# Optimization experiments

Hardware: AMD Instinct MI355X
Metric: run time of the kernel (lower is better)

## Reference

```python
import jax, jax.numpy as jnp
import numpy as np
import math

B, K, Q = 8, 3000, 256
KDIM = QDIM = ADIM = ODIM = 512
H_MA, H_CA = 4, 1
CHUNK = 16
SHARPEN = 1.0
EPS = 1e-6
INIT_R = -4.0


def setup_inputs() -> dict:
    key = jax.random.key(0)
    ks = jax.random.split(key, 10)
    s = 0.02  # weight scale so sigmoid/softmax operate in a sane range
    return {
        "key": jax.random.normal(ks[0], (B, K, KDIM), jnp.float32),
        "query": jax.random.normal(ks[1], (B, Q, QDIM), jnp.float32),
        "w_key_ma": jax.random.normal(ks[2], (KDIM, ADIM), jnp.float32) * s,
        "b_key_ma": jnp.zeros((ADIM,), jnp.float32),
        "w_query_ma": jax.random.normal(ks[3], (QDIM, ADIM), jnp.float32) * s,
        "b_query_ma": jnp.zeros((ADIM,), jnp.float32),
        "r": jnp.full((H_MA,), INIT_R, jnp.float32),
        "w_key_ca": jax.random.normal(ks[4], (KDIM, ADIM), jnp.float32) * s,
        "b_key_ca": jnp.zeros((ADIM,), jnp.float32),
        "w_query_ca": jax.random.normal(ks[5], (QDIM, ADIM), jnp.float32) * s,
        "b_query_ca": jnp.zeros((ADIM,), jnp.float32),
        "w_value": jax.random.normal(ks[6], (KDIM, ODIM), jnp.float32) * s,
        "b_value": jnp.zeros((ODIM,), jnp.float32),
    }


def _heads(x, n_heads):
    # [B, T, n_heads*d] -> [B, n_heads, T, d]
    b, t, d = x.shape
    return x.reshape(b, t, n_heads, d // n_heads).transpose(0, 2, 1, 3)


def moving_sum(x, back, forward):
    """Moving sum over last axis: out[k] = sum_{j=k-back}^{k+forward} x[j].
    Equivalent to F.conv1d with an all-ones kernel (cumsum-difference form)."""
    w = back + forward + 1
    pad = [(0, 0)] * (x.ndim - 1) + [(back, forward)]
    cs = jnp.cumsum(jnp.pad(x, pad), axis=-1)
    cs = jnp.concatenate([jnp.zeros_like(cs[..., :1]), cs], axis=-1)
    return cs[..., w:] - cs[..., :-w]


def exclusive_cumsum(x):
    # [a,b,c] -> [0,a,a+b] along last axis
    z = jnp.zeros_like(x[..., :1])
    return jnp.cumsum(jnp.concatenate([z, x[..., :-1]], axis=-1), axis=-1)


def safe_cumprod(x, eps):
    # exclusive cumprod via cumsum in log space
    return jnp.exp(exclusive_cumsum(jnp.log(jnp.clip(x, eps, 1.0))))


def monotonic_alpha(p_choose, eps):
    """Parallel (training-time) monotonic attention recurrence over qlen.
    p_choose: [B, H, Q, K] -> alpha: [B, H, Q, K]"""
    cp = safe_cumprod(1.0 - p_choose, eps)          # [B,H,Q,K]
    cp_c = jnp.clip(cp, eps, 1.0)
    # scan over query steps
    p_t = jnp.moveaxis(p_choose, 2, 0)              # [Q,B,H,K]
    cp_t = jnp.moveaxis(cp, 2, 0)
    cpc_t = jnp.moveaxis(cp_c, 2, 0)
    b, h, k = p_choose.shape[0], p_choose.shape[1], p_choose.shape[3]
    a0 = jnp.zeros((b, h, k), p_choose.dtype).at[:, :, 0].set(1.0)  # attend to frame 0

    def step(a_prev, inp):
        p_i, cp_i, cpc_i = inp
        a_i = p_i * cp_i * jnp.cumsum(a_prev / cpc_i, axis=-1)
        return a_i, a_i

    _, alpha_t = jax.lax.scan(step, a0, (p_t, cp_t, cpc_t))
    return jnp.moveaxis(alpha_t, 0, 2)              # [B,H,Q,K]


def efficient_chunkwise_attention(alpha, u, chunk_size, sharpening_factor):
    """alpha: [B,H_ma,Q,K], u: [B,H_ca,Q,K] (shared across MA heads).
    Returns beta: [B, H_ma*H_ca, Q, K]."""
    bs, h_ma, qlen, klen = alpha.shape
    a5 = alpha[:, :, None]                          # [B,H_ma,1,Q,K]
    u5 = u[:, None]                                 # [B,1,H_ca,Q,K]
    u5 = u5 - jnp.max(u5, axis=-1, keepdims=True)
    softmax_exp = jnp.clip(jnp.exp(u5), 1e-5, None)
    denom = moving_sum(softmax_exp, back=chunk_size - 1, forward=0)
    beta = softmax_exp * moving_sum(a5 * sharpening_factor / denom,
                                    back=0, forward=chunk_size - 1)
    return beta.reshape(bs, -1, qlen, klen)


def reference(key, query, w_key_ma, b_key_ma, w_query_ma, b_query_ma, r,
              w_key_ca, b_key_ca, w_query_ca, b_query_ca, w_value, b_value):
    scale = math.sqrt(ADIM)
    # monotonic energy (scaled_dot, H_ma heads) + offset r
    k_ma = _heads(key @ w_key_ma + b_key_ma, H_MA)          # [B,H,K,dk]
    q_ma = _heads(query @ w_query_ma + b_query_ma, H_MA)    # [B,H,Q,dk]
    e_ma = jnp.einsum('bhqd,bhkd->bhqk', q_ma, k_ma) / scale
    e_ma = e_ma + r[None, :, None, None]
    p_choose = jax.nn.sigmoid(e_ma)                          # [B,H_ma,Q,K]

    alpha = monotonic_alpha(p_choose, EPS)                   # [B,H_ma,Q,K]

    # chunk energy (scaled_dot, H_ca heads, shared across MA heads)
    k_ca = _heads(key @ w_key_ca + b_key_ca, H_CA)
    q_ca = _heads(query @ w_query_ca + b_query_ca, H_CA)
    u = jnp.einsum('bhqd,bhkd->bhqk', q_ca, k_ca) / scale    # [B,H_ca,Q,K]

    beta = efficient_chunkwise_attention(alpha, u, CHUNK, SHARPEN)  # [B,H_ma,Q,K]

    # context vector
    v = _heads(key @ w_value + b_value, H_MA * H_CA)         # [B,H,K,dv]
    cv = jnp.einsum('bhqk,bhkd->bhqd', beta, v)              # [B,H,Q,dv]
    cv = cv.transpose(0, 2, 1, 3).reshape(B, Q, ODIM)
    return cv, alpha, beta
```

## Files before the change

kernel.cpp:

```cpp
#include <hip/hip_runtime.h>
#include <hip/hip_bf16.h>
#include <math.h>

#define EPSV 1e-6f
#define INV_SCALE 0.04419417382415922f

typedef _Float16 half_t;
typedef __attribute__((ext_vector_type(8))) _Float16 half8;
typedef __attribute__((ext_vector_type(4))) _Float16 half4v;
typedef __attribute__((ext_vector_type(4))) float    f32x4;

__device__ __forceinline__ float ldf(const float* p)  { return *p; }
__device__ __forceinline__ float ldf(const half_t* p) { return (float)*p; }
__device__ __forceinline__ void  stf(float* p, float v)  { *p = v; }
__device__ __forceinline__ void  stf(half_t* p, float v) { *p = (half_t)v; }
__device__ __forceinline__ float frcp(float x) { return __builtin_amdgcn_rcpf(x); }
__device__ __forceinline__ half8 hz8() {
  half8 v = {(_Float16)0,(_Float16)0,(_Float16)0,(_Float16)0,
             (_Float16)0,(_Float16)0,(_Float16)0,(_Float16)0};
  return v;
}

template<int CTRL, int RMASK>
__device__ __forceinline__ float dpp_add_step(float x) {
  int t = __builtin_amdgcn_update_dpp(0, __float_as_int(x), CTRL, RMASK, 0xf, true);
  return x + __int_as_float(t);
}
template<int CTRL, int RMASK>
__device__ __forceinline__ float dpp_mul_step(float x) {
  int t = __builtin_amdgcn_update_dpp(0x3f800000, __float_as_int(x), CTRL, RMASK, 0xf, false);
  return x * __int_as_float(t);
}
__device__ __forceinline__ float wave_iscan_add(float x) {
  x = dpp_add_step<0x111,0xf>(x);
  x = dpp_add_step<0x112,0xf>(x);
  x = dpp_add_step<0x114,0xf>(x);
  x = dpp_add_step<0x118,0xf>(x);
  x = dpp_add_step<0x142,0xa>(x);
  x = dpp_add_step<0x143,0xc>(x);
  return x;
}
__device__ __forceinline__ float wave_iscan_mul(float x) {
  x = dpp_mul_step<0x111,0xf>(x);
  x = dpp_mul_step<0x112,0xf>(x);
  x = dpp_mul_step<0x114,0xf>(x);
  x = dpp_mul_step<0x118,0xf>(x);
  x = dpp_mul_step<0x142,0xa>(x);
  x = dpp_mul_step<0x143,0xc>(x);
  return x;
}

__device__ __forceinline__ void block_sync_lds() {
  asm volatile("s_waitcnt lgkmcnt(0)" ::: "memory");
  __builtin_amdgcn_s_barrier();
  asm volatile("" ::: "memory");
}

__device__ __forceinline__ float cross_sum4(const float* ws, int wid) {
  f32x4 a = *(const f32x4*)ws;
  float s = 0.f;
  #pragma unroll
  for (int j = 0; j < 4; j++) s += (wid > j) ? a[j] : 0.f;
  return s;
}
__device__ __forceinline__ float cross_prod4(const float* ws, int wid) {
  f32x4 a = *(const f32x4*)ws;
  float p = 1.f;
  #pragma unroll
  for (int j = 0; j < 4; j++) p *= (wid > j) ? a[j] : 1.f;
  return p;
}

__global__ __launch_bounds__(256)
void wtrans_all(const float* __restrict__ s0, half_t* __restrict__ d0,
                const float* __restrict__ s1, half_t* __restrict__ d1,
                const float* __restrict__ s2, half_t* __restrict__ d2,
                const float* __restrict__ s3, half_t* __restrict__ d3,
                const float* __restrict__ s4, half_t* __restrict__ d4)
{
  __shared__ float t[32][33];
  const float* W; half_t* WT;
  switch (blockIdx.z) {
    case 0: W = s0; WT = d0; break;
    case 1: W = s1; WT = d1; break;
    case 2: W = s2; WT = d2; break;
    case 3: W = s3; WT = d3; break;
    default: W = s4; WT = d4; break;
  }
  int bx = blockIdx.x, by = blockIdx.y;
  int tid = threadIdx.x;
  int r = tid >> 3, cq = tid & 7;
  float4 v = *(const float4*)&W[(size_t)(bx * 32 + r) * 512 + by * 32 + cq * 4];
  t[r][cq * 4 + 0] = v.x; t[r][cq * 4 + 1] = v.y;
  t[r][cq * 4 + 2] = v.z; t[r][cq * 4 + 3] = v.w;
  __syncthreads();
  half4v o;
  o[0] = (half_t)t[cq * 4 + 0][r];
  o[1] = (half_t)t[cq * 4 + 1][r];
  o[2] = (half_t)t[cq * 4 + 2][r];
  o[3] = (half_t)t[cq * 4 + 3][r];
  *(half4v*)&WT[(size_t)(by * 32 + r) * 512 + bx * 32 + cq * 4] = o;
}

__global__ __launch_bounds__(256)
void key2h(const float* __restrict__ in, half_t* __restrict__ out)
{
  int i = blockIdx.x * 256 + threadIdx.x;
  if (i < 3072000) {
    f32x4 v = *(const f32x4*)&in[(size_t)i * 4];
    half4v h;
    h[0] = (half_t)v[0]; h[1] = (half_t)v[1]; h[2] = (half_t)v[2]; h[3] = (half_t)v[3];
    *(half4v*)&out[(size_t)i * 4] = h;
  }
}

__global__ __launch_bounds__(256)
void catbias(const float* __restrict__ a, const float* __restrict__ b,
             const float* __restrict__ c, const float* __restrict__ d,
             float* __restrict__ cbq, float* __restrict__ cbk)
{
  int t = threadIdx.x;
  for (int i = t; i < 512; i += 256) {
    cbq[i] = a[i]; cbq[512 + i] = b[i];
    cbk[i] = c[i]; cbk[512 + i] = d[i];
  }
}

struct GemmLds { half_t As[4][128][8]; half_t Bs[4][128][8]; };
struct __align__(16) ScanLds { float wsA[2][4]; float wsB[2][4]; };

__device__ __forceinline__
void stage_a(GemmLds& L, int tid, const float* __restrict__ A,
             int M, int Ke, int lda, int m0, int k0)
{
  #pragma unroll
  for (int i = 0; i < 4; i++) {
    int ch = tid + i * 256;
    int m = ch >> 3, cq = ch & 7, k = cq * 4;
    float4 v = make_float4(0.f, 0.f, 0.f, 0.f);
    if (m0 + m < M && k0 + k < Ke) v = *(const float4*)&A[(size_t)(m0 + m) * lda + k0 + k];
    half4v h;
    h[0] = (half_t)v.x; h[1] = (half_t)v.y; h[2] = (half_t)v.z; h[3] = (half_t)v.w;
    *(half4v*)&L.As[cq >> 1][m][(cq & 1) * 4] = h;
  }
}
__device__ __forceinline__
void stage_a(GemmLds& L, int tid, const half_t* __restrict__ A,
             int M, int Ke, int lda, int m0, int k0)
{
  #pragma unroll
  for (int i = 0; i < 2; i++) {
    int ch = tid + i * 256;
    int m = ch >> 2, kb = ch & 3;
    half8 v = hz8();
    if (m0 + m < M && k0 + kb * 8 < Ke)
      v = *(const half8*)&A[(size_t)(m0 + m) * lda + k0 + kb * 8];
    *(half8*)&L.As[kb][m][0] = v;
  }
}

template<int MODE, bool CT, bool ATOM, typename TA, typename TC>
__device__ __forceinline__
void mgemm_body(GemmLds& L, int tid, int bxx, int byy, int bzz,
                const TA* __restrict__ A, const half_t* __restrict__ BT,
                TC* __restrict__ C, int M, int N, int Kd,
                int lda, int ldb, int ldc, int hdiv, int kdiv, int kc,
                long long sAb, long long sAh, long long sBb, long long sBh,
                long long sCb, long long sCh,
                const float* __restrict__ bias, const float* __restrict__ rvec)
{
  int ks = bzz % kdiv; int zz = bzz / kdiv;
  int bz = zz / hdiv, hz = zz - bz * hdiv;
  A  += (size_t)bz * sAb + (size_t)hz * sAh + (size_t)ks * kc;
  BT += (size_t)bz * sBb + (size_t)hz * sBh + (size_t)ks * kc;
  C  += (size_t)bz * sCb + (size_t)hz * sCh;
  int Ke = Kd - ks * kc; if (Ke > kc) Ke = kc;

  int lane = tid & 63, wid = tid >> 6;
  int wm = wid >> 1, wn = wid & 1;
  int m0 = byy * 128, n0 = bxx * 128;

  f32x4 acc[4][4] = {};

  for (int k0 = 0; k0 < Ke; k0 += 32) {
    stage_a(L, tid, A, M, Ke, lda, m0, k0);
    #pragma unroll
    for (int i = 0; i < 2; i++) {
      int ch = tid + i * 256;
      int n = ch >> 2, kb = ch & 3;
      half8 v = hz8();
      if (n0 + n < N && k0 + kb * 8 < Ke)
        v = *(const half8*)&BT[(size_t)(n0 + n) * ldb + k0 + kb * 8];
      *(half8*)&L.Bs[kb][n][0] = v;
    }
    __syncthreads();
    int kb = lane >> 4, r = lane & 15;
    half8 af[4], bfv[4];
    #pragma unroll
    for (int mi = 0; mi < 4; mi++) af[mi]  = *(const half8*)&L.As[kb][wm * 64 + mi * 16 + r][0];
    #pragma unroll
    for (int ni = 0; ni < 4; ni++) bfv[ni] = *(const half8*)&L.Bs[kb][wn * 64 + ni * 16 + r][0];
    #pragma unroll
    for (int mi = 0; mi < 4; mi++)
      #pragma unroll
      for (int ni = 0; ni < 4; ni++)
        acc[mi][ni] = __builtin_amdgcn_mfma_f32_16x16x32_f16(af[mi], bfv[ni], acc[mi][ni], 0, 0, 0);
    __syncthreads();
  }

  float radd = (MODE == 1) ? rvec[hz] : 0.f;
  int r = lane & 15, g = lane >> 4;
  #pragma unroll
  for (int mi = 0; mi < 4; mi++) {
    #pragma unroll
    for (int ni = 0; ni < 4; ni++) {
      int col = n0 + wn * 64 + ni * 16 + r;
      if (col >= N) continue;
      float bv = (MODE == 0) ? bias[col] : 0.f;
      if (CT) {
        int row0 = m0 + wm * 64 + mi * 16 + g * 4;
        if (row0 + 3 < M) {
          half4v o;
          #pragma unroll
          for (int j = 0; j < 4; j++) o[j] = (half_t)(acc[mi][ni][j] + bv);
          *(half4v*)&((half_t*)C)[(size_t)col * ldc + row0] = o;
        }
      } else {
        #pragma unroll
        for (int j = 0; j < 4; j++) {
          int row = m0 + wm * 64 + mi * 16 + g * 4 + j;
          if (row >= M) continue;
          float v = acc[mi][ni][j];
          if (MODE == 0)      v += bv;
          else if (MODE == 1) v = frcp(1.f + expf(-(v * INV_SCALE + radd)));
          else if (MODE == 2) v *= INV_SCALE;
          if (ATOM) atomicAdd((float*)&C[(size_t)row * ldc + col], v);
          else      stf(&C[(size_t)row * ldc + col], v);
        }
      }
    }
  }
}

template<int MODE, bool CT, bool ATOM, typename TA, typename TC>
__global__ __launch_bounds__(256)
void mgemm(const TA* __restrict__ A, const half_t* __restrict__ BT,
           TC* __restrict__ C, int M, int N, int Kd,
           int lda, int ldb, int ldc, int hdiv, int kdiv, int kc,
           long long sAb, long long sAh, long long sBb, long long sBh,
           long long sCb, long long sCh,
           const float* __restrict__ bias, const float* __restrict__ rvec)
{
  __shared__ GemmLds L;
  mgemm_body<MODE,CT,ATOM,TA,TC>(L, threadIdx.x, blockIdx.x, blockIdx.y, blockIdx.z,
                                 A, BT, C, M, N, Kd, lda, ldb, ldc, hdiv, kdiv, kc,
                                 sAb, sAh, sBb, sBh, sCb, sCh, bias, rvec);
}

union MidLds { GemmLds g; ScanLds s; };

__global__ __launch_bounds__(256, 1)
void fused_mid(const half_t* __restrict__ p16, float* __restrict__ alpha_slot,
               const half_t* __restrict__ qa, const half_t* __restrict__ kb,
               int lda_u, int ldb_u, long long sAb_u, long long sBb_u,
               float* __restrict__ u_buf,
               const half_t* __restrict__ keyh, const half_t* __restrict__ wt_v,
               half_t* __restrict__ vtbuf, const float* __restrict__ b_value)
{
  __shared__ MidLds lds;
  int blk = blockIdx.x;
  int tid = threadIdx.x;

  if (blk >= 32) {
    if (blk < 416) {
      int vb = blk - 32;
      int bx = vb % 24; int t = vb / 24;
      int by = t & 1;   int bz = t >> 1;
      mgemm_body<2,false,false,half_t,float>(lds.g, tid, bx, by, bz, qa, kb, u_buf,
          256, 3000, 512, lda_u, ldb_u, 3000, 1, 1, 512,
          sAb_u, 0, sBb_u, 0, 768000, 0, nullptr, nullptr);
    } else {
      int vb = blk - 416;
      int bx = vb & 3; int by = vb >> 2;
      mgemm_body<0,true,false,half_t,half_t>(lds.g, tid, bx, by, 0, keyh, wt_v, vtbuf,
          24000, 512, 512, 512, 512, 24000, 1, 1, 512,
          0, 0, 0, 0, 0, 0, b_value, nullptr);
    }
    return;
  }

  __builtin_amdgcn_s_setprio(1);
  float (&wsA)[2][4] = lds.s.wsA;
  float (&wsB)[2][4] = lds.s.wsB;
  int lane = tid & 63, wid = tid >> 6;
  int k0 = tid * 12;
  size_t zbase = (size_t)blk * 768000;
  const half_t* prow = p16 + zbase;

  half4v ph0[3], pb0[3], pb1[3], pb2[3], pb3[3], pb4[3], pb5[3], pb6[3], pb7[3];
  #pragma unroll
  for (int j = 0; j < 3; j++) {
    int k = k0 + j * 4;
    half4v z = {(_Float16)0,(_Float16)0,(_Float16)0,(_Float16)0};
    bool ok = (k + 4 <= 3000);
    ph0[j] = ok ? *(const half4v*)&prow[k]         : z;
    pb0[j] = ok ? *(const half4v*)&prow[3000 + k]  : z;
    pb1[j] = ok ? *(const half4v*)&prow[6000 + k]  : z;
    pb2[j] = ok ? *(const half4v*)&prow[9000 + k]  : z;
    pb3[j] = ok ? *(const half4v*)&prow[12000 + k] : z;
    pb4[j] = ok ? *(const half4v*)&prow[15000 + k] : z;
    pb5[j] = ok ? *(const half4v*)&prow[18000 + k] : z;
    pb6[j] = ok ? *(const half4v*)&prow[21000 + k] : z;
    pb7[j] = ok ? *(const half4v*)&prow[24000 + k] : z;
  }

  float a_prev[12];
  #pragma unroll
  for (int c = 0; c < 12; c++) a_prev[c] = 0.f;
  if (tid == 0) a_prev[0] = 1.f;

  float cpv[12], w[12];
  {
    float l[12], m = 1.f;
    float p0f[12];
    #pragma unroll
    for (int c = 0; c < 12; c++) {
      p0f[c] = (float)ph0[c >> 2][c & 3];
      l[c] = m;
      m *= fmaxf(1.f - p0f[c], EPSV);
    }
    float incl = wave_iscan_mul(m);
    if (lane == 63) wsA[1][wid] = incl;
    float exclw = incl * frcp(fmaxf(m, 1e-30f));
    block_sync_lds();
    float base = exclw * cross_prod4(&wsA[1][0], wid);
    #pragma unroll
    for (int c = 0; c < 12; c++) { cpv[c] = base * l[c]; w[c] = p0f[c] * cpv[c]; }
  }

#define SCAN_STEP(I, BUF)                                                     \
  {                                                                           \
    int par = (I) & 1;                                                        \
    float t_[12], s2 = 0.f;                                                   \
    _Pragma("unroll")                                                         \
    for (int c = 0; c < 12; c++) {                                            \
      s2 = fmaf(a_prev[c], frcp(fmaxf(cpv[c], EPSV)), s2);                    \
      t_[c] = s2;                                                             \
    }                                                                         \
    float incl2 = wave_iscan_add(s2);                                         \
    if (lane == 63) wsB[par][wid] = incl2;                                    \
    float excl2 = incl2 - s2;                                                 \
    float pnf[12], l_[12], m_ = 1.f;                                          \
    _Pragma("unroll")                                                         \
    for (int c = 0; c < 12; c++) {                                            \
      pnf[c] = (float)BUF[c >> 2][c & 3];                                     \
      l_[c] = m_;                                                             \
      m_ *= fmaxf(1.f - pnf[c], EPSV);                                        \
    }                                                                         \
    float incl1 = wave_iscan_mul(m_);                                         \
    if (lane == 63) wsA[par][wid] = incl1;                                    \
    float excl1 = incl1 * frcp(fmaxf(m_, 1e-30f));                            \
    block_sync_lds();                                                         \
    if ((I) + 9 <= 255) {                                                     \
      const half_t* nrow = prow + (size_t)((I) + 9) * 3000;                   \
      _Pragma("unroll")                                                       \
      for (int j = 0; j < 3; j++) {                                           \
        int k = k0 + j * 4;                                                   \
        if (k + 4 <= 3000) BUF[j] = *(const half4v*)&nrow[k];                 \
      }                                                                       \
    }                                                                         \
    __builtin_amdgcn_sched_barrier(0);                                        \
    float off = excl2 + cross_sum4(&wsB[par][0], wid);                        \
    size_t rbase = zbase + (size_t)(I) * 3000;                                \
    _Pragma("unroll")                                                         \
    for (int q4 = 0; q4 < 3; q4++) {                                          \
      f32x4 o;                                                                \
      _Pragma("unroll")                                                       \
      for (int j = 0; j < 4; j++) {                                           \
        int c = q4 * 4 + j;                                                   \
        float an = w[c] * (off + t_[c]);                                      \
        a_prev[c] = an;                                                       \
        o[j] = an;                                                            \
      }                                                                       \
      int k = k0 + q4 * 4;                                                    \
      if (k + 4 <= 3000) *(f32x4*)&alpha_slot[rbase + k] = o;                 \
    }                                                                         \
    float base1 = excl1 * cross_prod4(&wsA[par][0], wid);                     \
    _Pragma("unroll")                                                         \
    for (int c = 0; c < 12; c++) { cpv[c] = base1 * l_[c]; w[c] = pnf[c] * cpv[c]; } \
  }

  for (int i = 0; i < 256; i += 8) {
    SCAN_STEP(i,     pb0);
    SCAN_STEP(i + 1, pb1);
    SCAN_STEP(i + 2, pb2);
    SCAN_STEP(i + 3, pb3);
    SCAN_STEP(i + 4, pb4);
    SCAN_STEP(i + 5, pb5);
    SCAN_STEP(i + 6, pb6);
    SCAN_STEP(i + 7, pb7);
  }
#undef SCAN_STEP
}

__global__ __launch_bounds__(256)
void beta_kernel(const float* __restrict__ ubuf, const float* __restrict__ alpha_slot,
                 float* __restrict__ beta_slot)
{
  __shared__ __align__(16) float se[3008];
  __shared__ __align__(16) float dn[3008];
  __shared__ __align__(16) float tt[3024];
  __shared__ float red[4];
  int bq = blockIdx.x;
  int b = bq >> 8, q = bq & 255;
  int tid = threadIdx.x;
  int lane = tid & 63, wid = tid >> 6;
  const float* urow = ubuf + (size_t)bq * 3000;
  float lmax = -3.0e38f;
  for (int c = tid; c < 750; c += 256) {
    f32x4 v = *(const f32x4*)&urow[c * 4];
    *(f32x4*)&se[c * 4] = v;
    lmax = fmaxf(lmax, fmaxf(fmaxf(v[0], v[1]), fmaxf(v[2], v[3])));
  }
  #pragma unroll
  for (int d = 32; d > 0; d >>= 1) lmax = fmaxf(lmax, __shfl_xor(lmax, d));
  if (lane == 0) red[wid] = lmax;
  __syncthreads();
  float umax = fmaxf(fmaxf(red[0], red[1]), fmaxf(red[2], red[3]));
  for (int c = tid; c < 750; c += 256) {
    f32x4 v = *(const f32x4*)&se[c * 4];
    #pragma unroll
    for (int j = 0; j < 4; j++) v[j] = fmaxf(expf(v[j] - umax), 1e-5f);
    *(f32x4*)&se[c * 4] = v;
  }
  if (tid < 24) tt[3000 + tid] = 0.f;
  __syncthreads();
  for (int k = tid; k < 3000; k += 256) {
    int lo = k - 15; if (lo < 0) lo = 0;
    float s = 0.f;
    for (int j = lo; j <= k; j++) s += se[j];
    dn[k] = s;
  }
  __syncthreads();
  for (int h = 0; h < 4; h++) {
    const float* arow = alpha_slot + ((size_t)((b * 4 + h) * 256 + q)) * 3000;
    for (int c = tid; c < 750; c += 256) {
      f32x4 a = *(const f32x4*)&arow[c * 4];
      f32x4 d = *(const f32x4*)&dn[c * 4];
      f32x4 o;
      #pragma unroll
      for (int j = 0; j < 4; j++) o[j] = a[j] * frcp(d[j]);
      *(f32x4*)&tt[c * 4] = o;
    }
    __syncthreads();
    float* brow = beta_slot + ((size_t)((b * 4 + h) * 256 + q)) * 3000;
    for (int c = tid; c < 750; c += 256) {
      f32x4 o;
      #pragma unroll
      for (int j = 0; j < 4; j++) {
        int k = c * 4 + j;
        float s = 0.f;
        #pragma unroll
        for (int w = 0; w < 16; w++) s += tt[k + w];
        o[j] = se[k] * s;
      }
      *(f32x4*)&brow[c * 4] = o;
    }
    __syncthreads();
  }
}

extern "C" void kernel_launch(void* const* d_in, const int* in_sizes, int n_in,
                              void* d_out, int out_size, void* d_ws, size_t ws_size,
                              hipStream_t stream)
{
  const float* key        = (const float*)d_in[0];
  const float* query      = (const float*)d_in[1];
  const float* w_key_ma   = (const float*)d_in[2];
  const float* b_key_ma   = (const float*)d_in[3];
  const float* w_query_ma = (const float*)d_in[4];
  const float* b_query_ma = (const float*)d_in[5];
  const float* rvec       = (const float*)d_in[6];
  const float* w_key_ca   = (const float*)d_in[7];
  const float* b_key_ca   = (const float*)d_in[8];
  const float* w_query_ca = (const float*)d_in[9];
  const float* b_query_ca = (const float*)d_in[10];
  const float* w_value    = (const float*)d_in[11];
  const float* b_value    = (const float*)d_in[12];

  float* out       = (float*)d_out;
  float* cv_out    = out;
  float* alpha_out = out + (size_t)1048576;
  float* beta_out  = alpha_out + (size_t)24576000;
  half_t* p16      = (half_t*)beta_out;
  half_t* keyh     = (half_t*)(beta_out + 12288000);

  dim3 blk(256);
  bool v3 = ws_size >= (size_t)109322240;

  hipMemsetAsync(cv_out, 0, (size_t)1048576 * sizeof(float), stream);

  if (v3) {
    half_t* kbuf2 = (half_t*)d_ws;
    half_t* qbuf  = (half_t*)((char*)d_ws + 49152000);
    float*  u_buf = (float*)((char*)d_ws + 57540608);
    half_t* vtbuf = (half_t*)((char*)d_ws + 82116608);
    half_t* wt_q  = (half_t*)((char*)d_ws + 106692608);
    half_t* wt_k  = (half_t*)((char*)d_ws + 107741184);
    half_t* wt_v  = (half_t*)((char*)d_ws + 108789760);
    float*  cb_q  = (float*)((char*)d_ws + 109314048);
    float*  cb_k  = (float*)((char*)d_ws + 109318144);

    wtrans_all<<<dim3(16,16,5), blk, 0, stream>>>(
        w_query_ma, wt_q, w_query_ca, wt_q + 262144,
        w_key_ma,   wt_k, w_key_ca,   wt_k + 262144,
        w_value,    wt_v);
    catbias<<<dim3(1), blk, 0, stream>>>(b_query_ma, b_query_ca, b_key_ma, b_key_ca, cb_q, cb_k);
    key2h<<<dim3(12000), blk, 0, stream>>>(key, keyh);

    mgemm<0,false,false,float ,half_t><<<dim3(8,16,1),  blk, 0, stream>>>(query, wt_q, qbuf, 2048, 1024, 512, 512,512,1024, 1,1,512, 0,0,0,0,0,0, cb_q, nullptr);
    mgemm<0,false,false,half_t,half_t><<<dim3(8,188,1), blk, 0, stream>>>(keyh,  wt_k, kbuf2, 24000,1024, 512, 512,512,1024, 1,1,512, 0,0,0,0,0,0, cb_k, nullptr);

    mgemm<1,false,false,half_t,half_t><<<dim3(24,2,32), blk, 0, stream>>>(qbuf, kbuf2, p16, 256,3000, 128, 1024,1024,3000, 4,1,128,
        262144,128, 3072000,128, 3072000,768000, nullptr, rvec);

    fused_mid<<<dim3(1168), blk, 0, stream>>>(p16, alpha_out,
        qbuf + 512, kbuf2 + 512, 1024, 1024, 262144, 3072000,
        u_buf, keyh, wt_v, vtbuf, b_value);

    beta_kernel<<<dim3(2048), blk, 0, stream>>>(u_buf, alpha_out, beta_out);

    mgemm<3,false,true,float,float><<<dim3(1,2,256), blk, 0, stream>>>(beta_out, vtbuf, cv_out, 256,128,3000, 3000,24000,512, 4,8,384,
        3072000,768000, 3000,3072000, 131072,128, nullptr, nullptr);
  } else {
    if (ws_size < (size_t)55967744) return;
    half_t* kbuf   = (half_t*)d_ws;
    half_t* qbuf   = (half_t*)((char*)d_ws + 24576000);
    float*  u_buf  = (float*)((char*)d_ws + 28770304);
    half_t* wt_qma = (half_t*)((char*)d_ws + 53346304);
    half_t* wt_kma = (half_t*)((char*)d_ws + 53870592);
    half_t* wt_qca = (half_t*)((char*)d_ws + 54394880);
    half_t* wt_kca = (half_t*)((char*)d_ws + 54919168);
    half_t* wt_v   = (half_t*)((char*)d_ws + 55443456);

    wtrans_all<<<dim3(16,16,5), blk, 0, stream>>>(
        w_query_ma, wt_qma, w_query_ca, wt_qca,
        w_key_ma,   wt_kma, w_key_ca,   wt_kca,
        w_value,    wt_v);
    key2h<<<dim3(12000), blk, 0, stream>>>(key, keyh);

    mgemm<0,false,false,float ,half_t><<<dim3(4,16,1),  blk, 0, stream>>>(query, wt_qma, qbuf, 2048, 512, 512, 512,512,512, 1,1,512, 0,0,0,0,0,0, b_query_ma, nullptr);
    mgemm<0,false,false,half_t,half_t><<<dim3(4,188,1), blk, 0, stream>>>(keyh,  wt_kma, kbuf, 24000,512, 512, 512,512,512, 1,1,512, 0,0,0,0,0,0, b_key_ma,   nullptr);
    mgemm<1,false,false,half_t,half_t><<<dim3(24,2,32), blk, 0, stream>>>(qbuf,  kbuf, p16, 256,3000, 128, 512,512,3000, 4,1,128,
        131072,128, 1536000,128, 3072000,768000, nullptr, rvec);

    mgemm<0,false,false,float ,half_t><<<dim3(4,16,1),  blk, 0, stream>>>(query, wt_qca, qbuf, 2048, 512, 512, 512,512,512, 1,1,512, 0,0,0,0,0,0, b_query_ca, nullptr);
    mgemm<0,false,false,half_t,half_t><<<dim3(4,188,1), blk, 0, stream>>>(keyh,  wt_kca, kbuf, 24000,512, 512, 512,512,512, 1,1,512, 0,0,0,0,0,0, b_key_ca,   nullptr);

    fused_mid<<<dim3(416), blk, 0, stream>>>(p16, alpha_out,
        qbuf, kbuf, 512, 512, 131072, 1536000,
        u_buf, keyh, wt_v, kbuf, b_value);

    mgemm<0,true,false,half_t,half_t><<<dim3(4,188,1), blk, 0, stream>>>(keyh, wt_v, kbuf, 24000,512, 512, 512,512,24000, 1,1,512, 0,0,0,0,0,0, b_value, nullptr);

    beta_kernel<<<dim3(2048), blk, 0, stream>>>(u_buf, alpha_out, beta_out);

    mgemm<3,false,true,float,float><<<dim3(1,2,256), blk, 0, stream>>>(beta_out, kbuf, cv_out, 256,128,3000, 3000,24000,512, 4,8,384,
        3072000,768000, 3000,3072000, 131072,128, nullptr, nullptr);
  }
}
```

Measured before the change: 497.9 us.

## Merge prep kernels, fuse Q/K projections, use sliding-window sums in beta

The weight transpose, key fp16 conversion and bias concatenation are merged into one prep launch. The query and key projection GEMMs are merged into a single launch of 1632 blocks. In beta_kernel each thread now handles 12 contiguous positions and computes the 16-wide moving sums with a running add/subtract over register buffers, replacing the per-element 16-term loops. This cuts launch overhead and the redundant LDS reads in the windowed sums, at the cost of higher register use and some idle threads, since only 250 of 256 are active.

```diff
diff --git a/kernel.cpp b/kernel.cpp
--- a/kernel.cpp
+++ b/kernel.cpp
@@ -72,57 +72,56 @@
 }
 
 __global__ __launch_bounds__(256)
-void wtrans_all(const float* __restrict__ s0, half_t* __restrict__ d0,
-                const float* __restrict__ s1, half_t* __restrict__ d1,
-                const float* __restrict__ s2, half_t* __restrict__ d2,
-                const float* __restrict__ s3, half_t* __restrict__ d3,
-                const float* __restrict__ s4, half_t* __restrict__ d4)
+void prep(const float* __restrict__ s0, half_t* __restrict__ d0,
+          const float* __restrict__ s1, half_t* __restrict__ d1,
+          const float* __restrict__ s2, half_t* __restrict__ d2,
+          const float* __restrict__ s3, half_t* __restrict__ d3,
+          const float* __restrict__ s4, half_t* __restrict__ d4,
+          const float* __restrict__ key, half_t* __restrict__ keyh,
+          const float* __restrict__ ba, const float* __restrict__ bb,
+          const float* __restrict__ bc, const float* __restrict__ bd,
+          float* __restrict__ cbq, float* __restrict__ cbk)
 {
   __shared__ float t[32][33];
-  const float* W; half_t* WT;
-  switch (blockIdx.z) {
-    case 0: W = s0; WT = d0; break;
-    case 1: W = s1; WT = d1; break;
-    case 2: W = s2; WT = d2; break;
-    case 3: W = s3; WT = d3; break;
-    default: W = s4; WT = d4; break;
-  }
-  int bx = blockIdx.x, by = blockIdx.y;
+  int blk = blockIdx.x;
   int tid = threadIdx.x;
-  int r = tid >> 3, cq = tid & 7;
-  float4 v = *(const float4*)&W[(size_t)(bx * 32 + r) * 512 + by * 32 + cq * 4];
-  t[r][cq * 4 + 0] = v.x; t[r][cq * 4 + 1] = v.y;
-  t[r][cq * 4 + 2] = v.z; t[r][cq * 4 + 3] = v.w;
-  __syncthreads();
-  half4v o;
-  o[0] = (half_t)t[cq * 4 + 0][r];
-  o[1] = (half_t)t[cq * 4 + 1][r];
-  o[2] = (half_t)t[cq * 4 + 2][r];
-  o[3] = (half_t)t[cq * 4 + 3][r];
-  *(half4v*)&WT[(size_t)(by * 32 + r) * 512 + bx * 32 + cq * 4] = o;
-}
-
-__global__ __launch_bounds__(256)
-void key2h(const float* __restrict__ in, half_t* __restrict__ out)
-{
-  int i = blockIdx.x * 256 + threadIdx.x;
-  if (i < 3072000) {
-    f32x4 v = *(const f32x4*)&in[(size_t)i * 4];
-    half4v h;
-    h[0] = (half_t)v[0]; h[1] = (half_t)v[1]; h[2] = (half_t)v[2]; h[3] = (half_t)v[3];
-    *(half4v*)&out[(size_t)i * 4] = h;
-  }
-}
-
-__global__ __launch_bounds__(256)
-void catbias(const float* __restrict__ a, const float* __restrict__ b,
-             const float* __restrict__ c, const float* __restrict__ d,
-             float* __restrict__ cbq, float* __restrict__ cbk)
-{
-  int t = threadIdx.x;
-  for (int i = t; i < 512; i += 256) {
-    cbq[i] = a[i]; cbq[512 + i] = b[i];
-    cbk[i] = c[i]; cbk[512 + i] = d[i];
+  if (blk < 1280) {
+    const float* W; half_t* WT;
+    switch (blk >> 8) {
+      case 0: W = s0; WT = d0; break;
+      case 1: W = s1; WT = d1; break;
+      case 2: W = s2; WT = d2; break;
+      case 3: W = s3; WT = d3; break;
+      default: W = s4; WT = d4; break;
+    }
+    int tile = blk & 255;
+    int bx = tile & 15, by = tile >> 4;
+    int r = tid >> 3, cq = tid & 7;
+    float4 v = *(const float4*)&W[(size_t)(bx * 32 + r) * 512 + by * 32 + cq * 4];
+    t[r][cq * 4 + 0] = v.x; t[r][cq * 4 + 1] = v.y;
+    t[r][cq * 4 + 2] = v.z; t[r][cq * 4 + 3] = v.w;
+    __syncthreads();
+    half4v o;
+    o[0] = (half_t)t[cq * 4 + 0][r];
+    o[1] = (half_t)t[cq * 4 + 1][r];
+    o[2] = (half_t)t[cq * 4 + 2][r];
+    o[3] = (half_t)t[cq * 4 + 3][r];
+    *(half4v*)&WT[(size_t)(by * 32 + r) * 512 + bx * 32 + cq * 4] = o;
+  } else if (blk < 13280) {
+    int i = (blk - 1280) * 256 + tid;
+    if (i < 3072000) {
+      f32x4 v = *(const f32x4*)&key[(size_t)i * 4];
+      half4v h;
+      h[0] = (half_t)v[0]; h[1] = (half_t)v[1]; h[2] = (half_t)v[2]; h[3] = (half_t)v[3];
+      *(half4v*)&keyh[(size_t)i * 4] = h;
+    }
+  } else {
+    if (cbq != nullptr) {
+      for (int i = tid; i < 512; i += 256) {
+        cbq[i] = ba[i]; cbq[512 + i] = bb[i];
+        cbk[i] = bc[i]; cbk[512 + i] = bd[i];
+      }
+    }
   }
 }
 
@@ -255,6 +254,26 @@
   mgemm_body<MODE,CT,ATOM,TA,TC>(L, threadIdx.x, blockIdx.x, blockIdx.y, blockIdx.z,
                                  A, BT, C, M, N, Kd, lda, ldb, ldc, hdiv, kdiv, kc,
                                  sAb, sAh, sBb, sBh, sCb, sCh, bias, rvec);
+}
+
+__global__ __launch_bounds__(256)
+void qk_fused(const float* __restrict__ query, const half_t* __restrict__ keyh,
+              const half_t* __restrict__ wt_q, const half_t* __restrict__ wt_k,
+              half_t* __restrict__ qbuf, half_t* __restrict__ kbuf2,
+              const float* __restrict__ cb_q, const float* __restrict__ cb_k)
+{
+  __shared__ GemmLds L;
+  int blk = blockIdx.x;
+  if (blk < 128) {
+    mgemm_body<0,false,false,float,half_t>(L, threadIdx.x, blk & 7, blk >> 3, 0,
+        query, wt_q, qbuf, 2048, 1024, 512, 512, 512, 1024, 1, 1, 512,
+        0, 0, 0, 0, 0, 0, cb_q, nullptr);
+  } else {
+    int vb = blk - 128;
+    mgemm_body<0,false,false,half_t,half_t>(L, threadIdx.x, vb % 8, vb / 8, 0,
+        keyh, wt_k, kbuf2, 24000, 1024, 512, 512, 512, 1024, 1, 1, 512,
+        0, 0, 0, 0, 0, 0, cb_k, nullptr);
+  }
 }
 
 union MidLds { GemmLds g; ScanLds s; };
@@ -409,12 +428,14 @@
 {
   __shared__ __align__(16) float se[3008];
   __shared__ __align__(16) float dn[3008];
-  __shared__ __align__(16) float tt[3024];
+  __shared__ __align__(16) float tt[3040];
   __shared__ float red[4];
   int bq = blockIdx.x;
   int b = bq >> 8, q = bq & 255;
   int tid = threadIdx.x;
   int lane = tid & 63, wid = tid >> 6;
+  int k0 = tid * 12;
+  bool act = (k0 < 3000);
   const float* urow = ubuf + (size_t)bq * 3000;
   float lmax = -3.0e38f;
   for (int c = tid; c < 750; c += 256) {
@@ -433,13 +454,24 @@
     for (int j = 0; j < 4; j++) v[j] = fmaxf(expf(v[j] - umax), 1e-5f);
     *(f32x4*)&se[c * 4] = v;
   }
-  if (tid < 24) tt[3000 + tid] = 0.f;
+  if (tid < 40) tt[3000 + tid] = 0.f;
   __syncthreads();
-  for (int k = tid; k < 3000; k += 256) {
-    int lo = k - 15; if (lo < 0) lo = 0;
-    float s = 0.f;
-    for (int j = lo; j <= k; j++) s += se[j];
-    dn[k] = s;
+  if (act) {
+    float sb[27];
+    #pragma unroll
+    for (int j = 0; j < 27; j++) {
+      int idx = k0 - 15 + j;
+      sb[j] = (idx >= 0) ? se[idx] : 0.f;
+    }
+    float wsum = 0.f;
+    #pragma unroll
+    for (int j = 0; j < 16; j++) wsum += sb[j];
+    dn[k0] = wsum;
+    #pragma unroll
+    for (int j = 1; j < 12; j++) {
+      wsum += sb[15 + j] - sb[j - 1];
+      dn[k0 + j] = wsum;
+    }
   }
   __syncthreads();
   for (int h = 0; h < 4; h++) {
@@ -454,17 +486,27 @@
     }
     __syncthreads();
     float* brow = beta_slot + ((size_t)((b * 4 + h) * 256 + q)) * 3000;
-    for (int c = tid; c < 750; c += 256) {
-      f32x4 o;
+    if (act) {
+      float tb[28];
       #pragma unroll
-      for (int j = 0; j < 4; j++) {
-        int k = c * 4 + j;
-        float s = 0.f;
+      for (int j = 0; j < 28; j++) tb[j] = tt[k0 + j];
+      float wv = 0.f;
+      #pragma unroll
+      for (int j = 0; j < 16; j++) wv += tb[j];
+      float outv[12];
+      outv[0] = se[k0] * wv;
+      #pragma unroll
+      for (int j = 1; j < 12; j++) {
+        wv += tb[15 + j] - tb[j - 1];
+        outv[j] = se[k0 + j] * wv;
+      }
+      #pragma unroll
+      for (int q4 = 0; q4 < 3; q4++) {
+        f32x4 o;
         #pragma unroll
-        for (int w = 0; w < 16; w++) s += tt[k + w];
-        o[j] = se[k] * s;
+        for (int j = 0; j < 4; j++) o[j] = outv[q4 * 4 + j];
+        *(f32x4*)&brow[k0 + q4 * 4] = o;
       }
-      *(f32x4*)&brow[c * 4] = o;
     }
     __syncthreads();
   }
@@ -511,15 +553,13 @@
     float*  cb_q  = (float*)((char*)d_ws + 109314048);
     float*  cb_k  = (float*)((char*)d_ws + 109318144);
 
-    wtrans_all<<<dim3(16,16,5), blk, 0, stream>>>(
+    prep<<<dim3(13281), blk, 0, stream>>>(
         w_query_ma, wt_q, w_query_ca, wt_q + 262144,
         w_key_ma,   wt_k, w_key_ca,   wt_k + 262144,
-        w_value,    wt_v);
-    catbias<<<dim3(1), blk, 0, stream>>>(b_query_ma, b_query_ca, b_key_ma, b_key_ca, cb_q, cb_k);
-    key2h<<<dim3(12000), blk, 0, stream>>>(key, keyh);
-
-    mgemm<0,false,false,float ,half_t><<<dim3(8,16,1),  blk, 0, stream>>>(query, wt_q, qbuf, 2048, 1024, 512, 512,512,1024, 1,1,512, 0,0,0,0,0,0, cb_q, nullptr);
-    mgemm<0,false,false,half_t,half_t><<<dim3(8,188,1), blk, 0, stream>>>(keyh,  wt_k, kbuf2, 24000,1024, 512, 512,512,1024, 1,1,512, 0,0,0,0,0,0, cb_k, nullptr);
+        w_value,    wt_v, key, keyh,
+        b_query_ma, b_query_ca, b_key_ma, b_key_ca, cb_q, cb_k);
+
+    qk_fused<<<dim3(1632), blk, 0, stream>>>(query, keyh, wt_q, wt_k, qbuf, kbuf2, cb_q, cb_k);
 
     mgemm<1,false,false,half_t,half_t><<<dim3(24,2,32), blk, 0, stream>>>(qbuf, kbuf2, p16, 256,3000, 128, 1024,1024,3000, 4,1,128,
         262144,128, 3072000,128, 3072000,768000, nullptr, rvec);
@@ -543,11 +583,11 @@
     half_t* wt_kca = (half_t*)((char*)d_ws + 54919168);
     half_t* wt_v   = (half_t*)((char*)d_ws + 55443456);
 
-    wtrans_all<<<dim3(16,16,5), blk, 0, stream>>>(
+    prep<<<dim3(13281), blk, 0, stream>>>(
         w_query_ma, wt_qma, w_query_ca, wt_qca,
         w_key_ma,   wt_kma, w_key_ca,   wt_kca,
-        w_value,    wt_v);
-    key2h<<<dim3(12000), blk, 0, stream>>>(key, keyh);
+        w_value,    wt_v, key, keyh,
+        nullptr, nullptr, nullptr, nullptr, nullptr, nullptr);
 
     mgemm<0,false,false,float ,half_t><<<dim3(4,16,1),  blk, 0, stream>>>(query, wt_qma, qbuf, 2048, 512, 512, 512,512,512, 1,1,512, 0,0,0,0,0,0, b_query_ma, nullptr);
     mgemm<0,false,false,half_t,half_t><<<dim3(4,188,1), blk, 0, stream>>>(keyh,  wt_kma, kbuf, 24000,512, 512, 512,512,512, 1,1,512, 0,0,0,0,0,0, b_key_ma,   nullptr);
```

Result: faster. 429.1 us (-13.8%).
